# Kernel tuning notes

Hardware: AMD Instinct MI355X
Metric: run time of the kernel (lower is better)

Reference implementation:

```python
import jax, jax.numpy as jnp
import numpy as np

B, C, Ci = 4, 256, 128
T, H, W = 16, 28, 28
EPS = 1e-5  # BatchNorm eps


def conv1x1(x, w, b):
    # 1x1x1 Conv3d == channel-mixing GEMM. x: (b,c,t,h,w), w: (o,c), b: (o,)
    return jnp.einsum('bcthw,oc->bothw', x, w) + b[None, :, None, None, None]


def pool2(x):
    # MaxPool3d(kernel_size=2, stride=2); all spatial dims are even here.
    b, c, t, h, w = x.shape
    return x.reshape(b, c, t // 2, 2, h // 2, 2, w // 2, 2).max(axis=(3, 5, 7))


def setup_inputs() -> dict:
    key = jax.random.key(0)
    ks = jax.random.split(key, 9)
    kaiming_in = (2.0 / C) ** 0.5   # kaiming_normal_ fan_in for 1x1 conv
    kaiming_mid = (2.0 / Ci) ** 0.5
    return {
        'x': jax.random.normal(ks[0], (B, C, T, H, W), jnp.float32),
        'w_g': jax.random.normal(ks[1], (Ci, C), jnp.float32) * kaiming_in,
        'b_g': jnp.zeros((Ci,), jnp.float32),
        'w_theta': jax.random.normal(ks[2], (Ci, C), jnp.float32) * kaiming_in,
        'b_theta': jnp.zeros((Ci,), jnp.float32),
        'w_phi': jax.random.normal(ks[3], (Ci, C), jnp.float32) * kaiming_in,
        'b_phi': jnp.zeros((Ci,), jnp.float32),
        'w_W': jax.random.normal(ks[4], (C, Ci), jnp.float32) * kaiming_mid,
        'b_W': jnp.zeros((C,), jnp.float32),
        'bn_gamma': 1.0 + 0.1 * jax.random.normal(ks[5], (C,), jnp.float32),
        'bn_beta': 0.1 * jax.random.normal(ks[6], (C,), jnp.float32),
        'bn_mean': 0.1 * jax.random.normal(ks[7], (C,), jnp.float32),
        'bn_var': jax.random.uniform(ks[8], (C,), jnp.float32, 0.5, 1.5),
    }


def reference(x, w_g, b_g, w_theta, b_theta, w_phi, b_phi, w_W, b_W,
              bn_gamma, bn_beta, bn_mean, bn_var):
    b = x.shape[0]
    # g/phi are sub-sampled (MaxPool3d(2)) -> M = N/8 keys
    g_x = pool2(conv1x1(x, w_g, b_g)).reshape(b, Ci, -1).transpose(0, 2, 1)    # (b, M, Ci)
    theta_x = conv1x1(x, w_theta, b_theta).reshape(b, Ci, -1).transpose(0, 2, 1)  # (b, N, Ci)
    phi_x = pool2(conv1x1(x, w_phi, b_phi)).reshape(b, Ci, -1)                # (b, Ci, M)
    f = jnp.einsum('bnc,bcm->bnm', theta_x, phi_x)                            # (b, N, M)
    attn = jax.nn.softmax(f, axis=-1)
    y = jnp.einsum('bnm,bmc->bnc', attn, g_x)                                 # (b, N, Ci)
    y = y.transpose(0, 2, 1).reshape(b, Ci, T, H, W)
    W_y = conv1x1(y, w_W, b_W)
    # BatchNorm3d (eval mode with running stats)
    scale = (bn_gamma / jnp.sqrt(bn_var + EPS))[None, :, None, None, None]
    W_y = (W_y - bn_mean[None, :, None, None, None]) * scale + bn_beta[None, :, None, None, None]
    return W_y + x
```

## Files before the change

### kernel.cpp

```cpp
#include <hip/hip_runtime.h>
#include <math.h>

typedef _Float16 f16;
typedef _Float16 f16x8 __attribute__((ext_vector_type(8)));
typedef float f32x4 __attribute__((ext_vector_type(4)));
typedef float f32x16 __attribute__((ext_vector_type(16)));

#define BB 4
#define CC 256
#define CI 128
#define NN 12544
#define MM 1568
#define TP 8
#define HP 14
#define WP 14

#define OFF_W3T 0u
#define OFF_WWH 196608u
#define OFF_B3  262144u
#define OFF_SC  263168u
#define OFF_OFB 264192u
#define OFF_XT  265216u
#define OFF_TPG (OFF_XT + 25690112u)
#define OFF_PHI (OFF_TPG + 38535168u)
#define OFF_G   (OFF_PHI + 1605632u)
#define OFF_Y   (OFF_G + 1605632u)
#define WS_NEED (OFF_Y + 12845056u)
#define OFF_Y1  OFF_XT
#define OFF_ML  (OFF_XT + 12845056u)

static __device__ __forceinline__ f32x4 mfma16(f16x8 a, f16x8 b, f32x4 c) {
    return __builtin_amdgcn_mfma_f32_16x16x32_f16(a, b, c, 0, 0, 0);
}
static __device__ __forceinline__ f32x16 mfma32(f16x8 a, f16x8 b, f32x16 c) {
    return __builtin_amdgcn_mfma_f32_32x32x16_f16(a, b, c, 0, 0, 0);
}
static __device__ __forceinline__ unsigned pkrtz(float a, float b) {
    auto h = __builtin_amdgcn_cvt_pkrtz(a, b);
    return __builtin_bit_cast(unsigned, h);
}

__global__ __launch_bounds__(256) void k_prep(
    const float* __restrict__ wg, const float* __restrict__ bg,
    const float* __restrict__ wth, const float* __restrict__ bth_,
    const float* __restrict__ wph, const float* __restrict__ bph,
    const float* __restrict__ wW, const float* __restrict__ bW,
    const float* __restrict__ gam, const float* __restrict__ bet,
    const float* __restrict__ mean, const float* __restrict__ var,
    f16* __restrict__ w3t, f16* __restrict__ wWh, f16* __restrict__ b3,
    float* __restrict__ sc, float* __restrict__ ofb) {
    int r = blockIdx.x;
    int c = threadIdx.x;
    const float* src = (r < 128) ? (wth + (size_t)r * CC)
                     : (r < 256) ? (wph + (size_t)(r - 128) * CC)
                                 : (wg + (size_t)(r - 256) * CC);
    w3t[(size_t)r * CC + c] = (f16)src[c];
    if (c == 0) {
        float bv = (r < 128) ? bth_[r] : (r < 256) ? bph[r - 128] : bg[r - 256];
        b3[r] = (f16)bv;
    }
    if (r < 256) {
        if (c < 128) wWh[(size_t)r * CI + c] = (f16)wW[(size_t)r * CI + c];
        if (c == 0) {
            float s = gam[r] * rsqrtf(var[r] + 1e-5f);
            sc[r] = s;
            ofb[r] = (bW[r] - mean[r]) * s + bet[r];
        }
    }
}

__global__ __launch_bounds__(256) void k_xt(const float* __restrict__ x, f16* __restrict__ xT) {
    int bid = blockIdx.x;
    int b = bid / (196 * 4); int rem = bid % (196 * 4);
    int nt = rem / 4, ct = rem % 4;
    int n0 = nt * 64, c0 = ct * 64;
    __shared__ float tile[64][65];
    const float* xb = x + (size_t)b * CC * NN;
    for (int p = 0; p < 16; ++p) {
        int idx = p * 256 + threadIdx.x;
        int i = idx >> 6, j = idx & 63;
        tile[i][j] = xb[(size_t)(c0 + i) * NN + n0 + j];
    }
    __syncthreads();
    f16* xTb = xT + (size_t)b * NN * CC;
    for (int p = 0; p < 16; ++p) {
        int idx = p * 256 + threadIdx.x;
        int n = idx >> 6, c = idx & 63;
        xTb[(size_t)(n0 + n) * CC + c0 + c] = (f16)tile[c][n];
    }
}

__global__ __launch_bounds__(256) void k_conv(const f16* __restrict__ xT, const f16* __restrict__ w3t,
                                              const f16* __restrict__ b3, f16* __restrict__ tpg) {
    int bid = blockIdx.x;
    int b = bid / (98 * 3); int rem = bid % (98 * 3);
    int nt = rem / 3, ct = rem % 3;
    int n0 = nt * 128, co0 = ct * 128;
    __shared__ f16 As[128 * 64];
    __shared__ f16 Bs[128 * 64];
    const f16* xb = xT + (size_t)b * NN * CC + (size_t)n0 * CC;
    const f16* wb = w3t + (size_t)co0 * CC;
    int wv = threadIdx.x >> 6, ln = threadIdx.x & 63;
    int wr = (wv & 1) * 64, wc = (wv >> 1) * 64;
    f32x4 acc[4][4];
    for (int i = 0; i < 4; ++i) for (int j = 0; j < 4; ++j)
        for (int r = 0; r < 4; ++r) acc[i][j][r] = 0.f;
    for (int ks = 0; ks < 4; ++ks) {
        for (int s = threadIdx.x; s < 1024; s += 256) {
            int row = s >> 3, sl = s & 7;
            f16x8 va = *(const f16x8*)(xb + (size_t)row * CC + ks * 64 + sl * 8);
            *(f16x8*)(As + row * 64 + ((sl * 8) ^ ((row & 7) << 3))) = va;
            f16x8 vb = *(const f16x8*)(wb + (size_t)row * CC + ks * 64 + sl * 8);
            *(f16x8*)(Bs + row * 64 + ((sl * 8) ^ ((row & 7) << 3))) = vb;
        }
        __syncthreads();
        for (int kc = 0; kc < 2; ++kc) {
            int klo = kc * 32 + ((ln >> 4) * 8);
            f16x8 af[4], bf[4];
            for (int i = 0; i < 4; ++i) {
                int rn = wr + i * 16 + (ln & 15);
                af[i] = *(const f16x8*)(As + rn * 64 + (klo ^ ((rn & 7) << 3)));
                int rc = wc + i * 16 + (ln & 15);
                bf[i] = *(const f16x8*)(Bs + rc * 64 + (klo ^ ((rc & 7) << 3)));
            }
            for (int i = 0; i < 4; ++i)
                for (int j = 0; j < 4; ++j)
                    acc[i][j] = mfma16(af[i], bf[j], acc[i][j]);
        }
        __syncthreads();
    }
    f16* ob = tpg + (size_t)b * NN * 384 + (size_t)n0 * 384 + co0;
    for (int j = 0; j < 4; ++j) {
        float bias = (float)b3[co0 + wc + j * 16 + (ln & 15)];
        for (int i = 0; i < 4; ++i)
            for (int r = 0; r < 4; ++r) {
                int n = wr + i * 16 + (ln >> 4) * 4 + r;
                int co = wc + j * 16 + (ln & 15);
                ob[(size_t)n * 384 + co] = (f16)(acc[i][j][r] + bias);
            }
    }
}

__global__ __launch_bounds__(256) void k_pool(const f16* __restrict__ tpg,
                                              f16* __restrict__ phi, f16* __restrict__ gx) {
    int bid = blockIdx.x;
    int b = bid / (TP * HP); int rem = bid % (TP * HP);
    int tp = rem / HP, hp = rem % HP;
    const f16* base = tpg + (size_t)b * NN * 384;
    for (int idx = threadIdx.x; idx < WP * 128; idx += 256) {
        int wp = idx >> 7, ci = idx & 127;
        f16 mp = (f16)(-60000.0f), mg = (f16)(-60000.0f);
        for (int dt = 0; dt < 2; ++dt)
            for (int dh = 0; dh < 2; ++dh)
                for (int dw = 0; dw < 2; ++dw) {
                    int n = (2 * tp + dt) * 784 + (2 * hp + dh) * 28 + (2 * wp + dw);
                    f16 vp = base[(size_t)n * 384 + 128 + ci];
                    f16 vg = base[(size_t)n * 384 + 256 + ci];
                    mp = vp > mp ? vp : mp;
                    mg = vg > mg ? vg : mg;
                }
        int m = tp * 196 + hp * 14 + wp;
        phi[(size_t)b * MM * CI + (size_t)m * CI + ci] = mp;
        gx[(size_t)b * CI * MM + (size_t)ci * MM + m] = mg;
    }
}


template<int S>
__device__ __forceinline__ void stage_load(const f16* __restrict__ phib, const f16* __restrict__ gb,
                                           int m0, int tid, f16x8* sp, f16x8* sg) {
    #pragma unroll
    for (int p = 0; p < S / 16; ++p) {
        int s = p * 256 + tid;
        int row = s >> 4, sl = s & 15;
        sp[p] = *(const f16x8*)(phib + (size_t)(m0 + row) * CI + sl * 8);
    }
    #pragma unroll
    for (int p = 0; p < S / 16; ++p) {
        int s = p * 256 + tid;
        int row = (S == 64) ? (s >> 3) : (s >> 2);
        int sl  = (S == 64) ? (s & 7) : (s & 3);
        sg[p] = *(const f16x8*)(gb + (size_t)row * MM + m0 + sl * 8);
    }
}

template<int S>
__device__ __forceinline__ void stage_write(f16* __restrict__ Bp, f16* __restrict__ Bg,
                                            int tid, const f16x8* sp, const f16x8* sg) {
    #pragma unroll
    for (int p = 0; p < S / 16; ++p) {
        int s = p * 256 + tid;
        int row = s >> 4, sl = s & 15;
        *(f16x8*)(Bp + row * 128 + ((sl * 8) ^ ((row & 15) << 3))) = sp[p];
    }
    #pragma unroll
    for (int p = 0; p < S / 16; ++p) {
        int s = p * 256 + tid;
        int row = (S == 64) ? (s >> 3) : (s >> 2);
        int sl  = (S == 64) ? (s & 7) : (s & 3);
        *(f16x8*)(Bg + row * 64 + ((sl * 8) ^ ((row & 7) << 3))) = sg[p];
    }
}

template<int KF>
__device__ __forceinline__ void attn_chunk(const f16* __restrict__ Bp, const f16* __restrict__ Bg,
                                           const f16x8* bth, f32x16* yv,
                                           float& mrun, float& lrun, int lq, int hi) {
    f32x16 qk[KF];
    __builtin_amdgcn_s_setprio(1);
    #pragma unroll
    for (int kf = 0; kf < KF; ++kf) {
        #pragma unroll
        for (int r = 0; r < 16; ++r) qk[kf][r] = 0.f;
        int row = kf * 32 + lq;
        const f16* rp = Bp + row * 128;
        int sw = (row & 15) << 3;
        #pragma unroll
        for (int ks = 0; ks < 8; ++ks)
            qk[kf] = mfma32(*(const f16x8*)(rp + ((ks * 16 + hi * 8) ^ sw)), bth[ks], qk[kf]);
    }
    __builtin_amdgcn_s_setprio(0);
    float t[8];
    #pragma unroll
    for (int i = 0; i < 8; ++i) {
        t[i] = fmaxf(qk[0][i], qk[0][i + 8]);
        if (KF == 2) t[i] = fmaxf(t[i], fmaxf(qk[KF - 1][i], qk[KF - 1][i + 8]));
    }
    #pragma unroll
    for (int s = 4; s >= 1; s >>= 1)
        #pragma unroll
        for (int i = 0; i < s; ++i) t[i] = fmaxf(t[i], t[i + s]);
    float mx = fmaxf(t[0], __shfl_xor(t[0], 32));
    if (__any(mx > mrun + 8.f)) {
        float mnew = fmaxf(mrun, mx);
        float scl = __expf(mrun - mnew);
        lrun *= scl;
        #pragma unroll
        for (int c = 0; c < 4; ++c)
            #pragma unroll
            for (int r = 0; r < 16; ++r) yv[c][r] *= scl;
        mrun = mnew;
    }
    float ps = 0.f;
    #pragma unroll
    for (int kf = 0; kf < KF; ++kf)
        #pragma unroll
        for (int r = 0; r < 16; ++r) {
            float p = __expf(qk[kf][r] - mrun);
            qk[kf][r] = p;
            ps += p;
        }
    ps += __shfl_xor(ps, 32);
    lrun += ps;
    #pragma unroll
    for (int s = 0; s < 2 * KF; ++s) {
        const int kf = s >> 1;
        const int base = (s & 1) * 8;
        unsigned A0 = pkrtz(qk[kf][base + 0], qk[kf][base + 1]);
        unsigned A1 = pkrtz(qk[kf][base + 2], qk[kf][base + 3]);
        unsigned B0 = pkrtz(qk[kf][base + 4], qk[kf][base + 5]);
        unsigned B1 = pkrtz(qk[kf][base + 6], qk[kf][base + 7]);
        unsigned g0 = (unsigned)__shfl_xor((int)(hi ? A0 : B0), 32);
        unsigned g1 = (unsigned)__shfl_xor((int)(hi ? A1 : B1), 32);
        union { unsigned u[4]; f16x8 v; } fr;
        fr.u[0] = hi ? g0 : A0;
        fr.u[1] = hi ? g1 : A1;
        fr.u[2] = hi ? B0 : g0;
        fr.u[3] = hi ? B1 : g1;
        __builtin_amdgcn_s_setprio(1);
        #pragma unroll
        for (int c = 0; c < 4; ++c) {
            int row = c * 32 + lq;
            f16x8 gfr = *(const f16x8*)(Bg + row * 64 + ((s * 16 + hi * 8) ^ ((row & 7) << 3)));
            yv[c] = mfma32(gfr, fr.v, yv[c]);
        }
        __builtin_amdgcn_s_setprio(0);
    }
}

__global__ __launch_bounds__(256, 2) void k_attn(const f16* __restrict__ tpg, const f16* __restrict__ phi,
                                                 const f16* __restrict__ gx, f16* __restrict__ y0,
                                                 f16* __restrict__ y1, float2* __restrict__ ml) {
    int bid = blockIdx.x;
    int b = bid / 196; int rem = bid % 196;
    int nt = rem >> 1, kk = rem & 1;
    int n0 = nt * 128;
    __shared__ f16 Bp[64 * 128];
    __shared__ f16 Bg[128 * 64];
    int tid = threadIdx.x;
    int wv = tid >> 6, ln = tid & 63, hi = ln >> 5, lq = ln & 31;
    int n = n0 + wv * 32 + lq;
    f16x8 bth[8];
    {
        const f16* rowp = tpg + ((size_t)b * NN + n) * 384;
        #pragma unroll
        for (int ks = 0; ks < 8; ++ks)
            bth[ks] = *(const f16x8*)(rowp + ks * 16 + hi * 8);
    }
    f32x16 yv[4];
    #pragma unroll
    for (int c = 0; c < 4; ++c)
        #pragma unroll
        for (int r = 0; r < 16; ++r) yv[c][r] = 0.f;
    float mrun = -1e30f, lrun = 0.f;
    const f16* phib = phi + (size_t)b * MM * CI;
    const f16* gb = gx + (size_t)b * CI * MM;
    const int mbase = kk * 768;

    f16x8 sp[4], sg[4];
    stage_load<64>(phib, gb, mbase, tid, sp, sg);
    stage_write<64>(Bp, Bg, tid, sp, sg);
    __syncthreads();
    for (int t = 0; t < 12; ++t) {
        if (t < 11) stage_load<64>(phib, gb, mbase + (t + 1) * 64, tid, sp, sg);
        else if (kk == 0) stage_load<32>(phib, gb, 1536, tid, sp, sg);
        attn_chunk<2>(Bp, Bg, bth, yv, mrun, lrun, lq, hi);
        __syncthreads();
        if (t < 11) stage_write<64>(Bp, Bg, tid, sp, sg);
        else if (kk == 0) stage_write<32>(Bp, Bg, tid, sp, sg);
        __syncthreads();
    }
    if (kk == 0) attn_chunk<1>(Bp, Bg, bth, yv, mrun, lrun, lq, hi);

    float inv = 1.f / lrun;
    f16* yb = (kk ? y1 : y0) + ((size_t)b * NN + n) * CI;
    #pragma unroll
    for (int c = 0; c < 4; ++c)
        #pragma unroll
        for (int k = 0; k < 4; ++k) {
            int ci = c * 32 + k * 8 + hi * 4;
            uint2 st;
            st.x = pkrtz(yv[c][4 * k + 0] * inv, yv[c][4 * k + 1] * inv);
            st.y = pkrtz(yv[c][4 * k + 2] * inv, yv[c][4 * k + 3] * inv);
            *(uint2*)(yb + ci) = st;
        }
    if (hi == 0) {
        float2 v; v.x = mrun; v.y = lrun;
        ml[((size_t)b * 2 + kk) * NN + n] = v;
    }
}

__global__ __launch_bounds__(256) void k_out(const f16* __restrict__ wWh, const f16* __restrict__ y0,
                                             const f16* __restrict__ y1, const float2* __restrict__ ml,
                                             const float* __restrict__ x, const float* __restrict__ sc,
                                             const float* __restrict__ ofb, float* __restrict__ out) {
    int bid = blockIdx.x;
    int b = bid / (196 * 2); int rem = bid % (196 * 2);
    int nt = rem >> 1, ct = rem & 1;
    int n0 = nt * 64, co0 = ct * 128;
    __shared__ f16 Ws[128 * 128];
    __shared__ f16 Ys[64 * 128];
    for (int s = threadIdx.x; s < 128 * 16; s += 256) {
        int row = s >> 4, sl = s & 15;
        f16x8 v = *(const f16x8*)(wWh + (size_t)(co0 + row) * CI + sl * 8);
        *(f16x8*)(Ws + row * 128 + ((sl * 8) ^ ((row & 7) << 3))) = v;
    }
    const size_t ybase = (size_t)b * NN * CI + (size_t)n0 * CI;
    const float2* mlb = ml + (size_t)b * 2 * NN;
    for (int s = threadIdx.x; s < 64 * 16; s += 256) {
        int row = s >> 4, sl = s & 15;
        int n = n0 + row;
        float2 m0 = mlb[n];
        float2 m1 = mlb[NN + n];
        float M = fmaxf(m0.x, m1.x);
        float e0 = __expf(m0.x - M) * m0.y;
        float e1 = __expf(m1.x - M) * m1.y;
        float iL = 1.f / (e0 + e1);
        float w0 = e0 * iL, w1 = e1 * iL;
        f16x8 v0 = *(const f16x8*)(y0 + ybase + (size_t)row * CI + sl * 8);
        f16x8 v1 = *(const f16x8*)(y1 + ybase + (size_t)row * CI + sl * 8);
        union { unsigned u[4]; f16x8 v; } o;
        #pragma unroll
        for (int j = 0; j < 4; ++j)
            o.u[j] = pkrtz(w0 * (float)v0[2 * j] + w1 * (float)v1[2 * j],
                           w0 * (float)v0[2 * j + 1] + w1 * (float)v1[2 * j + 1]);
        *(f16x8*)(Ys + row * 128 + ((sl * 8) ^ ((row & 7) << 3))) = o.v;
    }
    __syncthreads();
    int wv = threadIdx.x >> 6, ln = threadIdx.x & 63;
    int wc = (wv >> 1) * 64, wn = (wv & 1) * 32;
    f32x4 acc[4][2];
    for (int i = 0; i < 4; ++i) for (int j = 0; j < 2; ++j)
        for (int r = 0; r < 4; ++r) acc[i][j][r] = 0.f;
    for (int kc = 0; kc < 4; ++kc) {
        int klo = kc * 32 + (ln >> 4) * 8;
        f16x8 afr[4], bfr[2];
        for (int i = 0; i < 4; ++i) {
            int rc = wc + i * 16 + (ln & 15);
            afr[i] = *(const f16x8*)(Ws + rc * 128 + (klo ^ ((rc & 7) << 3)));
        }
        for (int j = 0; j < 2; ++j) {
            int rn = wn + j * 16 + (ln & 15);
            bfr[j] = *(const f16x8*)(Ys + rn * 128 + (klo ^ ((rn & 7) << 3)));
        }
        for (int i = 0; i < 4; ++i)
            for (int j = 0; j < 2; ++j)
                acc[i][j] = mfma16(afr[i], bfr[j], acc[i][j]);
    }
    const float* xb = x + (size_t)b * CC * NN;
    float* ob = out + (size_t)b * CC * NN;
    for (int i = 0; i < 4; ++i)
        for (int j = 0; j < 2; ++j)
            for (int r = 0; r < 4; ++r) {
                int co = co0 + wc + i * 16 + (ln >> 4) * 4 + r;
                int n = n0 + wn + j * 16 + (ln & 15);
                size_t idx = (size_t)co * NN + n;
                ob[idx] = acc[i][j][r] * sc[co] + ofb[co] + xb[idx];
            }
}

extern "C" void kernel_launch(void* const* d_in, const int* in_sizes, int n_in,
                              void* d_out, int out_size, void* d_ws, size_t ws_size,
                              hipStream_t stream) {
    const float* x    = (const float*)d_in[0];
    const float* wg   = (const float*)d_in[1];
    const float* bg   = (const float*)d_in[2];
    const float* wth  = (const float*)d_in[3];
    const float* bth  = (const float*)d_in[4];
    const float* wph  = (const float*)d_in[5];
    const float* bph  = (const float*)d_in[6];
    const float* wW   = (const float*)d_in[7];
    const float* bW   = (const float*)d_in[8];
    const float* gam  = (const float*)d_in[9];
    const float* bet  = (const float*)d_in[10];
    const float* mean = (const float*)d_in[11];
    const float* var  = (const float*)d_in[12];
    if (ws_size < (size_t)WS_NEED) return;
    char* ws = (char*)d_ws;
    f16* w3t = (f16*)(ws + OFF_W3T);
    f16* wWh = (f16*)(ws + OFF_WWH);
    f16* b3  = (f16*)(ws + OFF_B3);
    float* sc  = (float*)(ws + OFF_SC);
    float* ofb = (float*)(ws + OFF_OFB);
    f16* xT  = (f16*)(ws + OFF_XT);
    f16* tpg = (f16*)(ws + OFF_TPG);
    f16* phi = (f16*)(ws + OFF_PHI);
    f16* gx  = (f16*)(ws + OFF_G);
    f16* yy0 = (f16*)(ws + OFF_Y);
    f16* yy1 = (f16*)(ws + OFF_Y1);
    float2* ml = (float2*)(ws + OFF_ML);
    float* out = (float*)d_out;

    k_prep<<<dim3(384), dim3(256), 0, stream>>>(wg, bg, wth, bth, wph, bph, wW, bW,
                                                gam, bet, mean, var, w3t, wWh, b3, sc, ofb);
    k_xt  <<<dim3(BB * 196 * 4), dim3(256), 0, stream>>>(x, xT);
    k_conv<<<dim3(BB * 98 * 3), dim3(256), 0, stream>>>(xT, w3t, b3, tpg);
    k_pool<<<dim3(BB * TP * HP), dim3(256), 0, stream>>>(tpg, phi, gx);
    k_attn<<<dim3(BB * 196), dim3(256), 0, stream>>>(tpg, phi, gx, yy0, yy1, ml);
    k_out <<<dim3(BB * 196 * 2), dim3(256), 0, stream>>>(wWh, yy0, yy1, ml, x, sc, ofb, out);
}
```

Measured before the change: 156.1 us.

## Drop LDS staging in attention kernel; read K/V fragments directly from global

The attention kernel no longer stages phi and g tiles through swizzled shared memory with double buffering and block barriers. Each single-wave block now loads its MFMA operands straight from global memory and relies on L1/L2 caching, with four times as many blocks. This removes the LDS writes and the __syncthreads overhead, but gives up K/V reuse across the four query waves of a block, so global and L2 traffic goes up. The per-lane strided 16-byte loads may also coalesce poorly.

```diff
diff --git a/kernel.cpp b/kernel.cpp
--- a/kernel.cpp
+++ b/kernel.cpp
@@ -166,44 +166,8 @@
 }
 
 
-template<int S>
-__device__ __forceinline__ void stage_load(const f16* __restrict__ phib, const f16* __restrict__ gb,
-                                           int m0, int tid, f16x8* sp, f16x8* sg) {
-    #pragma unroll
-    for (int p = 0; p < S / 16; ++p) {
-        int s = p * 256 + tid;
-        int row = s >> 4, sl = s & 15;
-        sp[p] = *(const f16x8*)(phib + (size_t)(m0 + row) * CI + sl * 8);
-    }
-    #pragma unroll
-    for (int p = 0; p < S / 16; ++p) {
-        int s = p * 256 + tid;
-        int row = (S == 64) ? (s >> 3) : (s >> 2);
-        int sl  = (S == 64) ? (s & 7) : (s & 3);
-        sg[p] = *(const f16x8*)(gb + (size_t)row * MM + m0 + sl * 8);
-    }
-}
-
-template<int S>
-__device__ __forceinline__ void stage_write(f16* __restrict__ Bp, f16* __restrict__ Bg,
-                                            int tid, const f16x8* sp, const f16x8* sg) {
-    #pragma unroll
-    for (int p = 0; p < S / 16; ++p) {
-        int s = p * 256 + tid;
-        int row = s >> 4, sl = s & 15;
-        *(f16x8*)(Bp + row * 128 + ((sl * 8) ^ ((row & 15) << 3))) = sp[p];
-    }
-    #pragma unroll
-    for (int p = 0; p < S / 16; ++p) {
-        int s = p * 256 + tid;
-        int row = (S == 64) ? (s >> 3) : (s >> 2);
-        int sl  = (S == 64) ? (s & 7) : (s & 3);
-        *(f16x8*)(Bg + row * 64 + ((sl * 8) ^ ((row & 7) << 3))) = sg[p];
-    }
-}
-
 template<int KF>
-__device__ __forceinline__ void attn_chunk(const f16* __restrict__ Bp, const f16* __restrict__ Bg,
+__device__ __forceinline__ void attn_chunk(const f16* __restrict__ pch, const f16* __restrict__ gch,
                                            const f16x8* bth, f32x16* yv,
                                            float& mrun, float& lrun, int lq, int hi) {
     f32x16 qk[KF];
@@ -212,12 +176,10 @@
     for (int kf = 0; kf < KF; ++kf) {
         #pragma unroll
         for (int r = 0; r < 16; ++r) qk[kf][r] = 0.f;
-        int row = kf * 32 + lq;
-        const f16* rp = Bp + row * 128;
-        int sw = (row & 15) << 3;
+        const f16* rp = pch + (size_t)(kf * 32) * CI;
         #pragma unroll
         for (int ks = 0; ks < 8; ++ks)
-            qk[kf] = mfma32(*(const f16x8*)(rp + ((ks * 16 + hi * 8) ^ sw)), bth[ks], qk[kf]);
+            qk[kf] = mfma32(*(const f16x8*)(rp + ks * 16), bth[ks], qk[kf]);
     }
     __builtin_amdgcn_s_setprio(0);
     float t[8];
@@ -270,26 +232,22 @@
         __builtin_amdgcn_s_setprio(1);
         #pragma unroll
         for (int c = 0; c < 4; ++c) {
-            int row = c * 32 + lq;
-            f16x8 gfr = *(const f16x8*)(Bg + row * 64 + ((s * 16 + hi * 8) ^ ((row & 7) << 3)));
+            f16x8 gfr = *(const f16x8*)(gch + (size_t)(c * 32) * MM + s * 16);
             yv[c] = mfma32(gfr, fr.v, yv[c]);
         }
         __builtin_amdgcn_s_setprio(0);
     }
 }
 
-__global__ __launch_bounds__(256, 2) void k_attn(const f16* __restrict__ tpg, const f16* __restrict__ phi,
-                                                 const f16* __restrict__ gx, f16* __restrict__ y0,
-                                                 f16* __restrict__ y1, float2* __restrict__ ml) {
+__global__ __launch_bounds__(64) void k_attn(const f16* __restrict__ tpg, const f16* __restrict__ phi,
+                                             const f16* __restrict__ gx, f16* __restrict__ y0,
+                                             f16* __restrict__ y1, float2* __restrict__ ml) {
     int bid = blockIdx.x;
-    int b = bid / 196; int rem = bid % 196;
-    int nt = rem >> 1, kk = rem & 1;
-    int n0 = nt * 128;
-    __shared__ f16 Bp[64 * 128];
-    __shared__ f16 Bg[128 * 64];
-    int tid = threadIdx.x;
-    int wv = tid >> 6, ln = tid & 63, hi = ln >> 5, lq = ln & 31;
-    int n = n0 + wv * 32 + lq;
+    int b = bid / 784; int rem = bid % 784;
+    int nt = rem >> 3; int sub = rem & 7;
+    int qw = sub >> 1, kk = sub & 1;
+    int ln = threadIdx.x, hi = ln >> 5, lq = ln & 31;
+    int n = nt * 128 + qw * 32 + lq;
     f16x8 bth[8];
     {
         const f16* rowp = tpg + ((size_t)b * NN + n) * 384;
@@ -303,24 +261,16 @@
         #pragma unroll
         for (int r = 0; r < 16; ++r) yv[c][r] = 0.f;
     float mrun = -1e30f, lrun = 0.f;
-    const f16* phib = phi + (size_t)b * MM * CI;
-    const f16* gb = gx + (size_t)b * CI * MM;
+    const f16* pbase = phi + (size_t)b * MM * CI + (size_t)lq * CI + hi * 8;
+    const f16* gbase = gx + (size_t)b * CI * MM + (size_t)lq * MM + hi * 8;
     const int mbase = kk * 768;
 
-    f16x8 sp[4], sg[4];
-    stage_load<64>(phib, gb, mbase, tid, sp, sg);
-    stage_write<64>(Bp, Bg, tid, sp, sg);
-    __syncthreads();
     for (int t = 0; t < 12; ++t) {
-        if (t < 11) stage_load<64>(phib, gb, mbase + (t + 1) * 64, tid, sp, sg);
-        else if (kk == 0) stage_load<32>(phib, gb, 1536, tid, sp, sg);
-        attn_chunk<2>(Bp, Bg, bth, yv, mrun, lrun, lq, hi);
-        __syncthreads();
-        if (t < 11) stage_write<64>(Bp, Bg, tid, sp, sg);
-        else if (kk == 0) stage_write<32>(Bp, Bg, tid, sp, sg);
-        __syncthreads();
-    }
-    if (kk == 0) attn_chunk<1>(Bp, Bg, bth, yv, mrun, lrun, lq, hi);
+        int m0 = mbase + t * 64;
+        attn_chunk<2>(pbase + (size_t)m0 * CI, gbase + m0, bth, yv, mrun, lrun, lq, hi);
+    }
+    if (kk == 0)
+        attn_chunk<1>(pbase + (size_t)1536 * CI, gbase + 1536, bth, yv, mrun, lrun, lq, hi);
 
     float inv = 1.f / lrun;
     f16* yb = (kk ? y1 : y0) + ((size_t)b * NN + n) * CI;
@@ -446,6 +396,6 @@
     k_xt  <<<dim3(BB * 196 * 4), dim3(256), 0, stream>>>(x, xT);
     k_conv<<<dim3(BB * 98 * 3), dim3(256), 0, stream>>>(xT, w3t, b3, tpg);
     k_pool<<<dim3(BB * TP * HP), dim3(256), 0, stream>>>(tpg, phi, gx);
-    k_attn<<<dim3(BB * 196), dim3(256), 0, stream>>>(tpg, phi, gx, yy0, yy1, ml);
+    k_attn<<<dim3(BB * 98 * 8), dim3(64), 0, stream>>>(tpg, phi, gx, yy0, yy1, ml);
     k_out <<<dim3(BB * 196 * 2), dim3(256), 0, stream>>>(wWh, yy0, yy1, ml, x, sc, ofb, out);
 }
```

After: 221.1 us. 41.7% more time.
